# Optimization experiments

Measured on AMD Instinct MI355X. Metric: run time of the kernel, lower is better.

## Reference

```python
import jax, jax.numpy as jnp
import numpy as np

NEG_BIG = -9e15
ALPHA = 0.2  # leakyrelu slope


def setup_inputs() -> dict:
    key = jax.random.key(0)
    k1, k2, k3, k4 = jax.random.split(key, 4)
    N, Fin, Fout = 8192, 256, 256
    input = jax.random.normal(k1, (N, Fin), dtype=jnp.float32)
    adj = jax.random.randint(k2, (N, N), 0, 2, dtype=jnp.int32)
    W = jax.random.normal(k3, (Fin, Fout), dtype=jnp.float32) * (1.0 / np.sqrt(Fin))
    a = jax.random.normal(k4, (2 * Fout, 1), dtype=jnp.float32) * (1.0 / np.sqrt(Fout))
    return {"input": input, "adj": adj, "W": W, "a": a}


def reference(input, adj, W, a):
    # h: [N, F]
    h = input @ W
    Fout = h.shape[1]
    # Fused score: e_ij = leakyrelu(h_i . a[:F] + h_j . a[F:])
    s1 = h @ a[:Fout, 0]   # [N]
    s2 = h @ a[Fout:, 0]   # [N]
    e = s1[:, None] + s2[None, :]            # [N, N]
    e = jnp.where(e >= 0, e, ALPHA * e)      # leaky relu
    e = jnp.where(adj > 0, e, NEG_BIG)       # mask
    attention = jax.nn.softmax(e, axis=1)    # row softmax
    h_prime = attention @ h                  # [N, F]
    return jax.nn.elu(h_prime)               # concat=True -> elu
```

## Files before the change

### kernel.cpp

```cpp
#include <hip/hip_runtime.h>
#include <hip/hip_bf16.h>

#define LRALPHA 0.2f

typedef __attribute__((ext_vector_type(8))) short frag_ab;
typedef __attribute__((ext_vector_type(4))) float frag_cd;
typedef int   iv4 __attribute__((ext_vector_type(4)));
typedef float fv4 __attribute__((ext_vector_type(4)));
typedef unsigned int uv4 __attribute__((ext_vector_type(4)));

static __device__ __forceinline__ unsigned short f2bf(float f) {
  __hip_bfloat16 b = __float2bfloat16(f);
  unsigned short u;
  __builtin_memcpy(&u, &b, 2);
  return u;
}

__global__ __launch_bounds__(256, 4) void gat_hproj(
    const float* __restrict__ X, const float* __restrict__ W,
    const float* __restrict__ avec,
    float* __restrict__ s1, float* __restrict__ s2,
    unsigned short* __restrict__ hT) {
  const int tid = threadIdx.x;
  const int row0 = blockIdx.x * 16;
  __shared__ __align__(16) float xs[16][256];
  const fv4* xsrc = (const fv4*)(X + (size_t)row0 * 256);
  fv4* xdst = (fv4*)&xs[0][0];
  for (int i = tid; i < 1024; i += 256) xdst[i] = xsrc[i];
  __syncthreads();

  const int c = tid;
  float acc[16];
#pragma unroll
  for (int r = 0; r < 16; ++r) acc[r] = 0.f;

  for (int k = 0; k < 256; k += 4) {
    const float w0 = W[(k + 0) * 256 + c];
    const float w1 = W[(k + 1) * 256 + c];
    const float w2 = W[(k + 2) * 256 + c];
    const float w3 = W[(k + 3) * 256 + c];
#pragma unroll
    for (int r = 0; r < 16; ++r) {
      const fv4 xv = *(const fv4*)&xs[r][k];
      acc[r] = fmaf(xv[0], w0, acc[r]);
      acc[r] = fmaf(xv[1], w1, acc[r]);
      acc[r] = fmaf(xv[2], w2, acc[r]);
      acc[r] = fmaf(xv[3], w3, acc[r]);
    }
  }

  alignas(16) unsigned short hu[16];
#pragma unroll
  for (int r = 0; r < 16; ++r) hu[r] = f2bf(acc[r]);
  uv4* hdst = (uv4*)(hT + (size_t)c * 8192 + row0);
  hdst[0] = *(const uv4*)&hu[0];
  hdst[1] = *(const uv4*)&hu[8];

  const float a1c = avec[c];
  const float a2c = avec[256 + c];
  const int lane = tid & 63, wave = tid >> 6;
  __shared__ float r1[4][16], r2[4][16];
#pragma unroll
  for (int r = 0; r < 16; ++r) {
    float v1 = acc[r] * a1c;
    float v2 = acc[r] * a2c;
#pragma unroll
    for (int off = 32; off > 0; off >>= 1) {
      v1 += __shfl_down(v1, off);
      v2 += __shfl_down(v2, off);
    }
    if (lane == 0) { r1[wave][r] = v1; r2[wave][r] = v2; }
  }
  __syncthreads();
  if (tid < 16) {
    s1[row0 + tid] = r1[0][tid] + r1[1][tid] + r1[2][tid] + r1[3][tid];
    s2[row0 + tid] = r2[0][tid] + r2[1][tid] + r2[2][tid] + r2[3][tid];
  }
}

__global__ void gat_s2max(const float* __restrict__ s2, float* __restrict__ s2max) {
  const int tid = threadIdx.x;
  float m = -1e30f;
  for (int i = tid; i < 8192; i += 256) m = fmaxf(m, s2[i]);
#pragma unroll
  for (int off = 32; off > 0; off >>= 1) m = fmaxf(m, __shfl_down(m, off));
  __shared__ float ws[4];
  if ((tid & 63) == 0) ws[tid >> 6] = m;
  __syncthreads();
  if (tid == 0) s2max[0] = fmaxf(fmaxf(ws[0], ws[1]), fmaxf(ws[2], ws[3]));
}

__global__ __launch_bounds__(512, 2) void gat_attn(
    const int* __restrict__ adj, const unsigned short* __restrict__ hT,
    const float* __restrict__ s1, const float* __restrict__ s2,
    const float* __restrict__ s2maxp,
    float* __restrict__ pacc, float* __restrict__ pZ) {
  const int bid = blockIdx.x;
  const int x = bid & 7;
  const int ks = x >> 2;
  const int rb = ((bid >> 3) << 2) | (x & 3);
  const int row0 = rb * 64;
  const int jlo = ks * 4096;
  const int tid = threadIdx.x;
  const int wave = tid >> 6, lane = tid & 63;
  const int ln16 = lane & 15, quad = lane >> 4;

  __shared__ __align__(16) unsigned short P[64][72];
  __shared__ float Zred[64][8];

  const int r = tid >> 3, cq = tid & 7;
  const float s1r = s1[row0 + r];
  const float s2m = s2maxp[0];
  const float tmv = s1r + s2m;
  const float mr = tmv >= 0.f ? tmv : LRALPHA * tmv;

  const int* adjRow = adj + (size_t)(row0 + r) * 8192 + jlo + cq * 8;
  const float* s2p = s2 + jlo + cq * 8;

  frag_cd acc[4][2];
  const frag_cd fz = {0.f, 0.f, 0.f, 0.f};
#pragma unroll
  for (int mi = 0; mi < 4; ++mi)
#pragma unroll
    for (int ni = 0; ni < 2; ++ni) acc[mi][ni] = fz;

  float zloc = 0.f;

  iv4 pa0 = __builtin_nontemporal_load((const iv4*)(adjRow));
  iv4 pa1 = __builtin_nontemporal_load((const iv4*)(adjRow + 4));
  fv4 pv0 = *(const fv4*)(s2p);
  fv4 pv1 = *(const fv4*)(s2p + 4);

  const int NIT = 4096 / 64;
  for (int jt = 0; jt < NIT; ++jt) {
    iv4 cav[2]; fv4 csv[2];
    cav[0] = pa0; cav[1] = pa1; csv[0] = pv0; csv[1] = pv1;
    if (jt + 1 < NIT) {
      const int o = (jt + 1) * 64;
      pa0 = __builtin_nontemporal_load((const iv4*)(adjRow + o));
      pa1 = __builtin_nontemporal_load((const iv4*)(adjRow + o + 4));
      pv0 = *(const fv4*)(s2p + o);
      pv1 = *(const fv4*)(s2p + o + 4);
    }

    alignas(16) unsigned short wv[8];
#pragma unroll
    for (int g = 0; g < 2; ++g) {
#pragma unroll
      for (int e = 0; e < 4; ++e) {
        float ee = s1r + csv[g][e];
        ee = ee >= 0.f ? ee : LRALPHA * ee;
        float w = __expf(ee - mr);
        w = cav[g][e] ? w : 0.f;
        const unsigned short u = f2bf(w);
        wv[g * 4 + e] = u;
        zloc += __uint_as_float((unsigned)u << 16);
      }
    }
    *(uv4*)&P[r][cq * 8] = *(const uv4*)wv;
    __syncthreads();

    const size_t jbase = (size_t)(jlo + jt * 64);
#pragma unroll
    for (int kk = 0; kk < 2; ++kk) {
      frag_ab af[4];
#pragma unroll
      for (int mi = 0; mi < 4; ++mi)
        af[mi] = *(const frag_ab*)&P[mi * 16 + ln16][kk * 32 + quad * 8];
      frag_ab bf[2];
#pragma unroll
      for (int ni = 0; ni < 2; ++ni) {
        const int f = wave * 32 + ni * 16 + ln16;
        bf[ni] = *(const frag_ab*)(hT + (size_t)f * 8192 + jbase + kk * 32 + quad * 8);
      }
#pragma unroll
      for (int mi = 0; mi < 4; ++mi)
#pragma unroll
        for (int ni = 0; ni < 2; ++ni)
          acc[mi][ni] = __builtin_amdgcn_mfma_f32_16x16x32_bf16(
              af[mi], bf[ni], acc[mi][ni], 0, 0, 0);
    }
    __syncthreads();
  }

  Zred[r][cq] = zloc;
  __syncthreads();
  if (tid < 64) {
    float z = 0.f;
#pragma unroll
    for (int q = 0; q < 8; ++q) z += Zred[tid][q];
    pZ[ks * 8192 + row0 + tid] = z;
  }

  float* paccb = pacc + ((size_t)ks * 8192 + row0) * 256;
#pragma unroll
  for (int mi = 0; mi < 4; ++mi) {
#pragma unroll
    for (int ni = 0; ni < 2; ++ni) {
      const int f = wave * 32 + ni * 16 + ln16;
#pragma unroll
      for (int reg = 0; reg < 4; ++reg) {
        const int grow = mi * 16 + quad * 4 + reg;
        __builtin_nontemporal_store(acc[mi][ni][reg], paccb + (size_t)grow * 256 + f);
      }
    }
  }
}

__global__ __launch_bounds__(256) void gat_combine(
    const float* __restrict__ pacc, const float* __restrict__ pZ,
    float* __restrict__ out) {
  const int idx = blockIdx.x * 256 + threadIdx.x;
  const int row = idx >> 6;
  const float z = pZ[row] + pZ[8192 + row];
  const float invz = 1.f / z;
  const fv4 n0 = *(const fv4*)(pacc + (size_t)idx * 4);
  const fv4 n1 = *(const fv4*)(pacc + 2097152 + (size_t)idx * 4);
  fv4 o;
#pragma unroll
  for (int e = 0; e < 4; ++e) {
    const float v = (n0[e] + n1[e]) * invz;
    o[e] = v > 0.f ? v : expm1f(v);
  }
  *(fv4*)(out + (size_t)idx * 4) = o;
}

extern "C" void kernel_launch(void* const* d_in, const int* in_sizes, int n_in,
                              void* d_out, int out_size, void* d_ws, size_t ws_size,
                              hipStream_t stream) {
  const float* X = (const float*)d_in[0];
  const int* adj = (const int*)d_in[1];
  const float* W = (const float*)d_in[2];
  const float* avec = (const float*)d_in[3];
  float* out = (float*)d_out;

  float* wsf = (float*)d_ws;
  float* s1 = wsf;
  float* s2 = wsf + 8192;
  float* s2m = wsf + 16384;
  float* pZ = wsf + 24576;
  float* pacc = wsf + 65536;
  unsigned short* hT = (unsigned short*)(wsf + 65536 + 4194304);

  hipLaunchKernelGGL(gat_hproj, dim3(512), dim3(256), 0, stream, X, W, avec, s1, s2, hT);
  hipLaunchKernelGGL(gat_s2max, dim3(1), dim3(256), 0, stream, s2, s2m);
  hipLaunchKernelGGL(gat_attn, dim3(256), dim3(512), 0, stream, adj, hT, s1, s2, s2m, pacc, pZ);
  hipLaunchKernelGGL(gat_combine, dim3(2048), dim3(256), 0, stream, pacc, pZ, out);
}
```

Baseline: 501.0 us.

## Split attention K into four parts and double-buffer the P tile

The attention kernel now splits the neighbor dimension into four 2048-column slices instead of two and launches 512 blocks with a higher occupancy target. A double-buffered shared P tile lets the next tile's weights be computed while MFMAs run on the current one, and hT fragments are loaded earlier. The projection kernel reads X straight from global memory instead of staging it in LDS, and bf16 rounding is done by hand. The aim is more parallelism and better overlap of the exp/mask math with the matrix math, at the cost of twice the partial-accumulator traffic in the combine step.

After: 487.0 us. 2.8% less time.

```diff
diff --git a/kernel.cpp b/kernel.cpp
--- a/kernel.cpp
+++ b/kernel.cpp
@@ -14,6 +14,27 @@
   unsigned short u;
   __builtin_memcpy(&u, &b, 2);
   return u;
+}
+
+static __device__ __forceinline__ uv4 make_w(const iv4* ca, const fv4* cv,
+                                             float s1r, float mr, float& zloc) {
+  alignas(16) unsigned short wv[8];
+#pragma unroll
+  for (int g = 0; g < 2; ++g) {
+#pragma unroll
+    for (int e = 0; e < 4; ++e) {
+      float ee = s1r + cv[g][e];
+      ee = fmaxf(ee, LRALPHA * ee);
+      float w = __expf(ee - mr);
+      w = ca[g][e] ? w : 0.f;
+      unsigned b = __float_as_uint(w);
+      b += 0x7FFFu + ((b >> 16) & 1u);
+      const unsigned short u = (unsigned short)(b >> 16);
+      wv[g * 4 + e] = u;
+      zloc += __uint_as_float((unsigned)u << 16);
+    }
+  }
+  return *(const uv4*)wv;
 }
 
 __global__ __launch_bounds__(256, 4) void gat_hproj(
@@ -23,13 +44,9 @@
     unsigned short* __restrict__ hT) {
   const int tid = threadIdx.x;
   const int row0 = blockIdx.x * 16;
-  __shared__ __align__(16) float xs[16][256];
-  const fv4* xsrc = (const fv4*)(X + (size_t)row0 * 256);
-  fv4* xdst = (fv4*)&xs[0][0];
-  for (int i = tid; i < 1024; i += 256) xdst[i] = xsrc[i];
-  __syncthreads();
-
+  const float* Xb = X + (size_t)row0 * 256;
   const int c = tid;
+
   float acc[16];
 #pragma unroll
   for (int r = 0; r < 16; ++r) acc[r] = 0.f;
@@ -41,11 +58,10 @@
     const float w3 = W[(k + 3) * 256 + c];
 #pragma unroll
     for (int r = 0; r < 16; ++r) {
-      const fv4 xv = *(const fv4*)&xs[r][k];
-      acc[r] = fmaf(xv[0], w0, acc[r]);
-      acc[r] = fmaf(xv[1], w1, acc[r]);
-      acc[r] = fmaf(xv[2], w2, acc[r]);
-      acc[r] = fmaf(xv[3], w3, acc[r]);
+      acc[r] = fmaf(Xb[r * 256 + k + 0], w0, acc[r]);
+      acc[r] = fmaf(Xb[r * 256 + k + 1], w1, acc[r]);
+      acc[r] = fmaf(Xb[r * 256 + k + 2], w2, acc[r]);
+      acc[r] = fmaf(Xb[r * 256 + k + 3], w3, acc[r]);
     }
   }
 
@@ -90,22 +106,22 @@
   if (tid == 0) s2max[0] = fmaxf(fmaxf(ws[0], ws[1]), fmaxf(ws[2], ws[3]));
 }
 
-__global__ __launch_bounds__(512, 2) void gat_attn(
+__global__ __launch_bounds__(512, 4) void gat_attn(
     const int* __restrict__ adj, const unsigned short* __restrict__ hT,
     const float* __restrict__ s1, const float* __restrict__ s2,
     const float* __restrict__ s2maxp,
     float* __restrict__ pacc, float* __restrict__ pZ) {
   const int bid = blockIdx.x;
   const int x = bid & 7;
-  const int ks = x >> 2;
-  const int rb = ((bid >> 3) << 2) | (x & 3);
+  const int ks = x >> 1;
+  const int rb = ((bid >> 3) << 1) | (x & 1);
   const int row0 = rb * 64;
-  const int jlo = ks * 4096;
+  const int jlo = ks * 2048;
   const int tid = threadIdx.x;
   const int wave = tid >> 6, lane = tid & 63;
   const int ln16 = lane & 15, quad = lane >> 4;
 
-  __shared__ __align__(16) unsigned short P[64][72];
+  __shared__ __align__(16) unsigned short P[2][64][72];
   __shared__ float Zred[64][8];
 
   const int r = tid >> 3, cq = tid & 7;
@@ -125,62 +141,64 @@
     for (int ni = 0; ni < 2; ++ni) acc[mi][ni] = fz;
 
   float zloc = 0.f;
-
-  iv4 pa0 = __builtin_nontemporal_load((const iv4*)(adjRow));
-  iv4 pa1 = __builtin_nontemporal_load((const iv4*)(adjRow + 4));
-  fv4 pv0 = *(const fv4*)(s2p);
-  fv4 pv1 = *(const fv4*)(s2p + 4);
-
-  const int NIT = 4096 / 64;
+  const int NIT = 2048 / 64;
+
+  {
+    iv4 ca[2]; fv4 cv[2];
+    ca[0] = __builtin_nontemporal_load((const iv4*)(adjRow));
+    ca[1] = __builtin_nontemporal_load((const iv4*)(adjRow + 4));
+    cv[0] = *(const fv4*)(s2p);
+    cv[1] = *(const fv4*)(s2p + 4);
+    *(uv4*)&P[0][r][cq * 8] = make_w(ca, cv, s1r, mr, zloc);
+  }
+  iv4 a[2]; fv4 v[2];
+  a[0] = __builtin_nontemporal_load((const iv4*)(adjRow + 64));
+  a[1] = __builtin_nontemporal_load((const iv4*)(adjRow + 68));
+  v[0] = *(const fv4*)(s2p + 64);
+  v[1] = *(const fv4*)(s2p + 68);
+  __syncthreads();
+
   for (int jt = 0; jt < NIT; ++jt) {
-    iv4 cav[2]; fv4 csv[2];
-    cav[0] = pa0; cav[1] = pa1; csv[0] = pv0; csv[1] = pv1;
+    const int cur = jt & 1, nxt = cur ^ 1;
+    const size_t jbase = (size_t)(jlo + jt * 64);
+
+    frag_ab bf[2][2];
+#pragma unroll
+    for (int kk = 0; kk < 2; ++kk)
+#pragma unroll
+      for (int ni = 0; ni < 2; ++ni) {
+        const int f = wave * 32 + ni * 16 + ln16;
+        bf[kk][ni] = *(const frag_ab*)(hT + (size_t)f * 8192 + jbase + kk * 32 + quad * 8);
+      }
+
+    iv4 a2[2]; fv4 v2[2];
+    if (jt + 2 < NIT) {
+      const int o = (jt + 2) * 64;
+      a2[0] = __builtin_nontemporal_load((const iv4*)(adjRow + o));
+      a2[1] = __builtin_nontemporal_load((const iv4*)(adjRow + o + 4));
+      v2[0] = *(const fv4*)(s2p + o);
+      v2[1] = *(const fv4*)(s2p + o + 4);
+    }
+
     if (jt + 1 < NIT) {
-      const int o = (jt + 1) * 64;
-      pa0 = __builtin_nontemporal_load((const iv4*)(adjRow + o));
-      pa1 = __builtin_nontemporal_load((const iv4*)(adjRow + o + 4));
-      pv0 = *(const fv4*)(s2p + o);
-      pv1 = *(const fv4*)(s2p + o + 4);
-    }
-
-    alignas(16) unsigned short wv[8];
-#pragma unroll
-    for (int g = 0; g < 2; ++g) {
-#pragma unroll
-      for (int e = 0; e < 4; ++e) {
-        float ee = s1r + csv[g][e];
-        ee = ee >= 0.f ? ee : LRALPHA * ee;
-        float w = __expf(ee - mr);
-        w = cav[g][e] ? w : 0.f;
-        const unsigned short u = f2bf(w);
-        wv[g * 4 + e] = u;
-        zloc += __uint_as_float((unsigned)u << 16);
-      }
-    }
-    *(uv4*)&P[r][cq * 8] = *(const uv4*)wv;
-    __syncthreads();
-
-    const size_t jbase = (size_t)(jlo + jt * 64);
+      *(uv4*)&P[nxt][r][cq * 8] = make_w(a, v, s1r, mr, zloc);
+    }
+
 #pragma unroll
     for (int kk = 0; kk < 2; ++kk) {
       frag_ab af[4];
 #pragma unroll
       for (int mi = 0; mi < 4; ++mi)
-        af[mi] = *(const frag_ab*)&P[mi * 16 + ln16][kk * 32 + quad * 8];
-      frag_ab bf[2];
-#pragma unroll
-      for (int ni = 0; ni < 2; ++ni) {
-        const int f = wave * 32 + ni * 16 + ln16;
-        bf[ni] = *(const frag_ab*)(hT + (size_t)f * 8192 + jbase + kk * 32 + quad * 8);
-      }
+        af[mi] = *(const frag_ab*)&P[cur][mi * 16 + ln16][kk * 32 + quad * 8];
 #pragma unroll
       for (int mi = 0; mi < 4; ++mi)
 #pragma unroll
         for (int ni = 0; ni < 2; ++ni)
           acc[mi][ni] = __builtin_amdgcn_mfma_f32_16x16x32_bf16(
-              af[mi], bf[ni], acc[mi][ni], 0, 0, 0);
+              af[mi], bf[kk][ni], acc[mi][ni], 0, 0, 0);
     }
     __syncthreads();
+    a[0] = a2[0]; a[1] = a2[1]; v[0] = v2[0]; v[1] = v2[1];
   }
 
   Zred[r][cq] = zloc;
@@ -212,15 +230,19 @@
     float* __restrict__ out) {
   const int idx = blockIdx.x * 256 + threadIdx.x;
   const int row = idx >> 6;
-  const float z = pZ[row] + pZ[8192 + row];
+  const float z = pZ[row] + pZ[8192 + row] + pZ[16384 + row] + pZ[24576 + row];
   const float invz = 1.f / z;
+  const size_t PSTRIDE = (size_t)8192 * 256;
   const fv4 n0 = *(const fv4*)(pacc + (size_t)idx * 4);
-  const fv4 n1 = *(const fv4*)(pacc + 2097152 + (size_t)idx * 4);
+  const fv4 n1 = *(const fv4*)(pacc + PSTRIDE + (size_t)idx * 4);
+  const fv4 n2 = *(const fv4*)(pacc + 2 * PSTRIDE + (size_t)idx * 4);
+  const fv4 n3 = *(const fv4*)(pacc + 3 * PSTRIDE + (size_t)idx * 4);
   fv4 o;
 #pragma unroll
   for (int e = 0; e < 4; ++e) {
-    const float v = (n0[e] + n1[e]) * invz;
-    o[e] = v > 0.f ? v : expm1f(v);
+    const float vsum = (n0[e] + n1[e]) + (n2[e] + n3[e]);
+    const float vv = vsum * invz;
+    o[e] = vv > 0.f ? vv : expm1f(vv);
   }
   *(fv4*)(out + (size_t)idx * 4) = o;
 }
@@ -240,10 +262,10 @@
   float* s2m = wsf + 16384;
   float* pZ = wsf + 24576;
   float* pacc = wsf + 65536;
-  unsigned short* hT = (unsigned short*)(wsf + 65536 + 4194304);
+  unsigned short* hT = (unsigned short*)(wsf + 65536 + 4 * 8192 * 256);
 
   hipLaunchKernelGGL(gat_hproj, dim3(512), dim3(256), 0, stream, X, W, avec, s1, s2, hT);
   hipLaunchKernelGGL(gat_s2max, dim3(1), dim3(256), 0, stream, s2, s2m);
-  hipLaunchKernelGGL(gat_attn, dim3(256), dim3(512), 0, stream, adj, hT, s1, s2, s2m, pacc, pZ);
+  hipLaunchKernelGGL(gat_attn, dim3(512), dim3(512), 0, stream, adj, hT, s1, s2, s2m, pacc, pZ);
   hipLaunchKernelGGL(gat_combine, dim3(2048), dim3(256), 0, stream, pacc, pZ, out);
 }
```
